# Kernel tuning notes

Hardware: AMD Instinct MI355X
Metric: run time of the kernel (lower is better)

Reference implementation:

```python
import jax, jax.numpy as jnp
import numpy as np

E, B, C, M, H = 8, 2, 1024, 2048, 7168


def setup_inputs() -> dict:
    key = jax.random.key(0)
    k1, k2, k3, k4 = jax.random.split(key, 4)
    # kaiming_uniform-ish scale for weights (bound = sqrt(6/fan_in)/sqrt(1+5) ~ 1/sqrt(fan_in))
    s_in = 1.0 / np.sqrt(M)
    s_ffn = 1.0 / np.sqrt(H)
    return {
        "dispatch_input": jax.random.normal(k1, (E, B, C, M), dtype=jnp.float32),
        "w1": jax.random.uniform(k2, (E, M, H), dtype=jnp.float32, minval=-s_in, maxval=s_in),
        "w2": jax.random.uniform(k3, (E, H, M), dtype=jnp.float32, minval=-s_ffn, maxval=s_ffn),
        "w3": jax.random.uniform(k4, (E, M, H), dtype=jnp.float32, minval=-s_in, maxval=s_in),
    }


def reference(dispatch_input, w1, w2, w3):
    # Batched per-expert SwiGLU MLP.
    # gate: [E,B,C,H], up: [E,B,C,H]
    gate = jnp.einsum("ebcm,emh->ebch", dispatch_input, w1)
    up = jnp.einsum("ebcm,emh->ebch", dispatch_input, w3)
    hidden = jax.nn.silu(gate) * up
    out = jnp.einsum("ebch,ehm->ebcm", hidden, w2)
    return out
```

## Files before the change

### kernel.cpp

```cpp
#include <hip/hip_runtime.h>

typedef __attribute__((ext_vector_type(8))) short bf16x8;
typedef __attribute__((ext_vector_type(4))) float f32x4;
typedef __attribute__((ext_vector_type(4))) unsigned int u32x4;
typedef __attribute__((ext_vector_type(4))) unsigned short u16x4;

#define NE 8
#define NT 2048
#define NM 2048
#define NH 7168

#define BAR() asm volatile("s_barrier" ::: "memory")
#define WAITV(N) asm volatile("s_waitcnt vmcnt(" #N ")" ::: "memory")

__device__ __forceinline__ unsigned short f2bf(float f) {
    unsigned int u = __float_as_uint(f);
    return (unsigned short)((u + 0x7fffu + ((u >> 16) & 1u)) >> 16);
}

__device__ __forceinline__ void gld16(const void* g, void* l) {
    __builtin_amdgcn_global_load_lds(
        (const __attribute__((address_space(1))) void*)g,
        (__attribute__((address_space(3))) void*)l, 16, 0, 0);
}


__global__ __launch_bounds__(256) void convert_x_kernel(
        const float* __restrict__ in, unsigned short* __restrict__ out) {
    const int i = blockIdx.x * 256 + threadIdx.x;
    f32x4 a = ((const f32x4*)in)[i];
    ((u16x4*)out)[i] = (u16x4){f2bf(a[0]), f2bf(a[1]), f2bf(a[2]), f2bf(a[3])};
}

__global__ __launch_bounds__(256) void convert_wT_kernel(
        const float* __restrict__ in, unsigned short* __restrict__ out,
        int R, int C) {
    const int t = threadIdx.x;
    const int e = blockIdx.y;
    const int tiles_c = C >> 6;
    const int tr = blockIdx.x / tiles_c, tc = blockIdx.x % tiles_c;

    const float* ip = in + (size_t)e * R * C + (size_t)(tr * 64) * C + tc * 64;
    unsigned short* op = out + (size_t)e * R * C + (size_t)(tc * 64) * R + tr * 64;

    __shared__ unsigned short tl[64][68];

    const int rr = t >> 4, c4 = (t & 15) * 4;
#pragma unroll
    for (int q = 0; q < 4; ++q) {
        const int r = q * 16 + rr;
        f32x4 v = *(const f32x4*)(ip + (size_t)r * C + c4);
        *(u16x4*)&tl[r][c4] = (u16x4){f2bf(v[0]), f2bf(v[1]), f2bf(v[2]), f2bf(v[3])};
    }
    __syncthreads();
#pragma unroll
    for (int q = 0; q < 4; ++q) {
        const int oc = q * 16 + rr;
        u16x4 v = (u16x4){tl[c4][oc], tl[c4 + 1][oc], tl[c4 + 2][oc], tl[c4 + 3][oc]};
        *(u16x4*)(op + (size_t)oc * R + c4) = v;
    }
}

__global__ __launch_bounds__(256) void convert_w13_kernel(
        const float* __restrict__ w1, const float* __restrict__ w3,
        unsigned short* __restrict__ wcat) {
    const int t = threadIdx.x;
    const int e = blockIdx.y;
    const int tiles_c = NH >> 6;
    const int tr = blockIdx.x / tiles_c, tc = blockIdx.x % tiles_c;

    __shared__ unsigned short tl[64][68];
    const int rr = t >> 4, c4 = (t & 15) * 4;
    unsigned short* ob = wcat + (size_t)e * (2 * NH) * NM + (size_t)(tc * 128) * NM + tr * 64;

#pragma unroll
    for (int pass = 0; pass < 2; ++pass) {
        const float* ip = (pass ? w3 : w1) + (size_t)e * NM * NH + (size_t)(tr * 64) * NH + tc * 64;
        if (pass) __syncthreads();
#pragma unroll
        for (int q = 0; q < 4; ++q) {
            const int r = q * 16 + rr;
            f32x4 v = *(const f32x4*)(ip + (size_t)r * NH + c4);
            *(u16x4*)&tl[r][c4] = (u16x4){f2bf(v[0]), f2bf(v[1]), f2bf(v[2]), f2bf(v[3])};
        }
        __syncthreads();
#pragma unroll
        for (int q = 0; q < 4; ++q) {
            const int oc = q * 16 + rr;
            const int orow = ((oc >> 4) * 32) + pass * 16 + (oc & 15);
            u16x4 v = (u16x4){tl[c4][oc], tl[c4 + 1][oc], tl[c4 + 2][oc], tl[c4 + 3][oc]};
            *(u16x4*)(ob + (size_t)orow * NM + c4) = v;
        }
    }
}

__global__ __launch_bounds__(512, 2) void gemm1p_kernel(
        const unsigned short* __restrict__ xb, const unsigned short* __restrict__ wcat,
        unsigned short* __restrict__ hid) {
    const int tid = threadIdx.x;
    const int lane = tid & 63, wv = tid >> 6;
    const int wr = wv >> 2, wc = wv & 3;
    const int e = blockIdx.y;
    const int d = blockIdx.x;
    const int l = (d & 7) * 56 + (d >> 3);
    const int ct = l >> 3, tt = l & 7;

    const unsigned short* ag = xb   + (size_t)(e * NT + tt * 256) * NM;
    const unsigned short* bg = wcat + (size_t)e * (2 * NH) * NM + (size_t)(ct * 256) * NM;
    unsigned short* hg = hid + (size_t)(e * NT + tt * 256) * NH + ct * 128;

    __shared__ __align__(16) unsigned short lds[2 * 32768];

    const int frow = lane & 15;
    const int fks  = (lane >> 4) * 8;
    const int la   = lane * 8;
    const int lr   = lane & 15, lq = lane >> 4;

    f32x4 acc[8][4];
#pragma unroll
    for (int m = 0; m < 8; ++m)
#pragma unroll
        for (int n = 0; n < 4; ++n) acc[m][n] = (f32x4){0.f, 0.f, 0.f, 0.f};

    auto stageA = [&](int t, int kh, int buf) {
        unsigned short* dst = lds + buf * 32768 + (kh * 16 + wv) * 512;
        const unsigned short* src = ag + (size_t)(wv * 16 + frow) * NM + t * 64 + kh * 32 + fks;
        gld16(src, dst);
        gld16(src + (size_t)128 * NM, dst + 8 * 512);
    };
    auto stageB = [&](int t, int kh, int buf) {
        unsigned short* dst = lds + buf * 32768 + 16384 + (kh * 16 + wv) * 512;
        const unsigned short* src = bg + (size_t)(wv * 16 + frow) * NM + t * 64 + kh * 32 + fks;
        gld16(src, dst);
        gld16(src + (size_t)128 * NM, dst + 8 * 512);
    };

    const int NKT = NM / 64;
    stageA(0, 0, 0); stageB(0, 0, 0); stageA(0, 1, 0); stageB(0, 1, 0);
    WAITV(4); BAR();

    for (int t = 0; t < NKT; ++t) {
        const int buf = t & 1, nb = buf ^ 1;
        const bool more = (t + 1 < NKT);
        const unsigned short* bA = lds + buf * 32768;
        const unsigned short* bB = bA + 16384;
        bf16x8 af[4], bfr[4];

#pragma unroll
        for (int m = 0; m < 4; ++m) af[m] = *(const bf16x8*)(bA + (wr * 8 + m) * 512 + la);
#pragma unroll
        for (int n = 0; n < 4; ++n) bfr[n] = *(const bf16x8*)(bB + (wc * 4 + n) * 512 + la);
        if (more) stageA(t + 1, 0, nb);
        BAR();
        __builtin_amdgcn_s_setprio(1);
#pragma unroll
        for (int m = 0; m < 4; ++m)
#pragma unroll
            for (int n = 0; n < 4; ++n)
                acc[m][n] = __builtin_amdgcn_mfma_f32_16x16x32_bf16(af[m], bfr[n], acc[m][n], 0, 0, 0);
        __builtin_amdgcn_s_setprio(0);
        BAR();

#pragma unroll
        for (int m = 0; m < 4; ++m) af[m] = *(const bf16x8*)(bA + (wr * 8 + 4 + m) * 512 + la);
        if (more) stageB(t + 1, 0, nb);
        BAR();
        __builtin_amdgcn_s_setprio(1);
#pragma unroll
        for (int m = 0; m < 4; ++m)
#pragma unroll
            for (int n = 0; n < 4; ++n)
                acc[4 + m][n] = __builtin_amdgcn_mfma_f32_16x16x32_bf16(af[m], bfr[n], acc[4 + m][n], 0, 0, 0);
        __builtin_amdgcn_s_setprio(0);
        if (more) { WAITV(4); } else { WAITV(0); }
        BAR();

#pragma unroll
        for (int m = 0; m < 4; ++m) af[m] = *(const bf16x8*)(bA + (16 + wr * 8 + m) * 512 + la);
#pragma unroll
        for (int n = 0; n < 4; ++n) bfr[n] = *(const bf16x8*)(bB + (16 + wc * 4 + n) * 512 + la);
        if (more) stageA(t + 1, 1, nb);
        BAR();
        __builtin_amdgcn_s_setprio(1);
#pragma unroll
        for (int m = 0; m < 4; ++m)
#pragma unroll
            for (int n = 0; n < 4; ++n)
                acc[m][n] = __builtin_amdgcn_mfma_f32_16x16x32_bf16(af[m], bfr[n], acc[m][n], 0, 0, 0);
        __builtin_amdgcn_s_setprio(0);
        BAR();

#pragma unroll
        for (int m = 0; m < 4; ++m) af[m] = *(const bf16x8*)(bA + (16 + wr * 8 + 4 + m) * 512 + la);
        if (more) stageB(t + 1, 1, nb);
        BAR();
        __builtin_amdgcn_s_setprio(1);
#pragma unroll
        for (int m = 0; m < 4; ++m)
#pragma unroll
            for (int n = 0; n < 4; ++n)
                acc[4 + m][n] = __builtin_amdgcn_mfma_f32_16x16x32_bf16(af[m], bfr[n], acc[4 + m][n], 0, 0, 0);
        __builtin_amdgcn_s_setprio(0);
        if (more) { WAITV(4); }
        BAR();
    }

#pragma unroll
    for (int mf = 0; mf < 8; ++mf)
#pragma unroll
        for (int p = 0; p < 2; ++p)
#pragma unroll
            for (int i = 0; i < 4; ++i) {
                const float g = acc[mf][2 * p][i];
                const float u = acc[mf][2 * p + 1][i];
                const float s = g / (1.f + __expf(-g));
                const int r = wr * 128 + mf * 16 + lq * 4 + i;
                const int h = wc * 32 + p * 16 + lr;
                hg[(size_t)r * NH + h] = f2bf(s * u);
            }
}

__global__ __launch_bounds__(512, 2) void gemm2p_kernel(
        const unsigned short* __restrict__ hid, const unsigned short* __restrict__ w2t,
        float* __restrict__ out) {
    const int tid = threadIdx.x;
    const int lane = tid & 63, wv = tid >> 6;
    const int wr = wv >> 2, wc = wv & 3;
    const int e = blockIdx.y;
    const int d = blockIdx.x;
    const int l = (d & 7) * 8 + (d >> 3);
    const int mt = l >> 3, tt = l & 7;

    const unsigned short* ag = hid + (size_t)(e * NT + tt * 256) * NH;
    const unsigned short* bg = w2t + (size_t)e * NM * NH + (size_t)(mt * 256) * NH;
    float* og = out + (size_t)(e * NT + tt * 256) * NM + mt * 256;

    __shared__ __align__(16) unsigned short lds[2 * 32768];

    const int frow = lane & 15;
    const int fks  = (lane >> 4) * 8;
    const int la   = lane * 8;
    const int lr   = lane & 15, lq = lane >> 4;

    f32x4 acc[8][4];
#pragma unroll
    for (int m = 0; m < 8; ++m)
#pragma unroll
        for (int n = 0; n < 4; ++n) acc[m][n] = (f32x4){0.f, 0.f, 0.f, 0.f};

    auto stageA = [&](int t, int kh, int buf) {
        unsigned short* dst = lds + buf * 32768 + (kh * 16 + wv) * 512;
        const unsigned short* src = ag + (size_t)(wv * 16 + frow) * NH + t * 64 + kh * 32 + fks;
        gld16(src, dst);
        gld16(src + (size_t)128 * NH, dst + 8 * 512);
    };
    auto stageB = [&](int t, int kh, int buf) {
        unsigned short* dst = lds + buf * 32768 + 16384 + (kh * 16 + wv) * 512;
        const unsigned short* src = bg + (size_t)(wv * 16 + frow) * NH + t * 64 + kh * 32 + fks;
        gld16(src, dst);
        gld16(src + (size_t)128 * NH, dst + 8 * 512);
    };

    const int NKT = NH / 64;
    stageA(0, 0, 0); stageB(0, 0, 0); stageA(0, 1, 0); stageB(0, 1, 0);
    WAITV(4); BAR();

    for (int t = 0; t < NKT; ++t) {
        const int buf = t & 1, nb = buf ^ 1;
        const bool more = (t + 1 < NKT);
        const unsigned short* bA = lds + buf * 32768;
        const unsigned short* bB = bA + 16384;
        bf16x8 af[4], bfr[4];

#pragma unroll
        for (int m = 0; m < 4; ++m) af[m] = *(const bf16x8*)(bA + (wr * 8 + m) * 512 + la);
#pragma unroll
        for (int n = 0; n < 4; ++n) bfr[n] = *(const bf16x8*)(bB + (wc * 4 + n) * 512 + la);
        if (more) stageA(t + 1, 0, nb);
        BAR();
        __builtin_amdgcn_s_setprio(1);
#pragma unroll
        for (int m = 0; m < 4; ++m)
#pragma unroll
            for (int n = 0; n < 4; ++n)
                acc[m][n] = __builtin_amdgcn_mfma_f32_16x16x32_bf16(af[m], bfr[n], acc[m][n], 0, 0, 0);
        __builtin_amdgcn_s_setprio(0);
        BAR();

#pragma unroll
        for (int m = 0; m < 4; ++m) af[m] = *(const bf16x8*)(bA + (wr * 8 + 4 + m) * 512 + la);
        if (more) stageB(t + 1, 0, nb);
        BAR();
        __builtin_amdgcn_s_setprio(1);
#pragma unroll
        for (int m = 0; m < 4; ++m)
#pragma unroll
            for (int n = 0; n < 4; ++n)
                acc[4 + m][n] = __builtin_amdgcn_mfma_f32_16x16x32_bf16(af[m], bfr[n], acc[4 + m][n], 0, 0, 0);
        __builtin_amdgcn_s_setprio(0);
        if (more) { WAITV(4); } else { WAITV(0); }
        BAR();

#pragma unroll
        for (int m = 0; m < 4; ++m) af[m] = *(const bf16x8*)(bA + (16 + wr * 8 + m) * 512 + la);
#pragma unroll
        for (int n = 0; n < 4; ++n) bfr[n] = *(const bf16x8*)(bB + (16 + wc * 4 + n) * 512 + la);
        if (more) stageA(t + 1, 1, nb);
        BAR();
        __builtin_amdgcn_s_setprio(1);
#pragma unroll
        for (int m = 0; m < 4; ++m)
#pragma unroll
            for (int n = 0; n < 4; ++n)
                acc[m][n] = __builtin_amdgcn_mfma_f32_16x16x32_bf16(af[m], bfr[n], acc[m][n], 0, 0, 0);
        __builtin_amdgcn_s_setprio(0);
        BAR();

#pragma unroll
        for (int m = 0; m < 4; ++m) af[m] = *(const bf16x8*)(bA + (16 + wr * 8 + 4 + m) * 512 + la);
        if (more) stageB(t + 1, 1, nb);
        BAR();
        __builtin_amdgcn_s_setprio(1);
#pragma unroll
        for (int m = 0; m < 4; ++m)
#pragma unroll
            for (int n = 0; n < 4; ++n)
                acc[4 + m][n] = __builtin_amdgcn_mfma_f32_16x16x32_bf16(af[m], bfr[n], acc[4 + m][n], 0, 0, 0);
        __builtin_amdgcn_s_setprio(0);
        if (more) { WAITV(4); }
        BAR();
    }

#pragma unroll
    for (int mf = 0; mf < 8; ++mf)
#pragma unroll
        for (int n = 0; n < 4; ++n)
#pragma unroll
            for (int i = 0; i < 4; ++i) {
                const int r = wr * 128 + mf * 16 + lq * 4 + i;
                const int c = wc * 64 + n * 16 + lr;
                og[(size_t)r * NM + c] = acc[mf][n][i];
            }
}

#define ROWB 80
#define TILEB (128 * ROWB)

__global__ __launch_bounds__(256, 2) void gemm1_fb_kernel(
        const float* __restrict__ x, const float* __restrict__ w1,
        const float* __restrict__ w3, unsigned short* __restrict__ hid) {
    const int tid = threadIdx.x;
    const int e = blockIdx.y;
    const int d = blockIdx.x;
    const int l = (d & 7) * 112 + (d >> 3);
    const int hn = l >> 4, tm = l & 15;

    const float* xg  = x  + (size_t)(e * NT + tm * 128) * NM;
    const float* w1g = w1 + (size_t)e * NM * NH + hn * 128;
    const float* w3g = w3 + (size_t)e * NM * NH + hn * 128;
    unsigned short* hg = hid + (size_t)(e * NT + tm * 128) * NH + hn * 128;

    __shared__ __align__(16) unsigned char lds[2 * 3 * TILEB];

    const int a_r = tid >> 3, a_c4 = tid & 7;
    const int w_kq = (tid >> 2) & 7;
    const int w_cg = ((tid >> 5) << 2) | (tid & 3);

    const int lane = tid & 63;
    const int wv = tid >> 6;
    const int r0w = (wv >> 1) * 64, c0w = (wv & 1) * 64;
    const int lr = lane & 15, lq = lane >> 4;

    f32x4 accg[4][4], accu[4][4];
#pragma unroll
    for (int m = 0; m < 4; ++m)
#pragma unroll
        for (int n = 0; n < 4; ++n) {
            accg[m][n] = (f32x4){0.f, 0.f, 0.f, 0.f};
            accu[m][n] = (f32x4){0.f, 0.f, 0.f, 0.f};
        }

    f32x4 la0, la1, la2, la3;
    f32x4 l10, l11, l12, l13, l30, l31, l32, l33;

    auto stage_load = [&](int ks) {
        const int k0 = ks * 32;
        const float* pa = xg + (size_t)a_r * NM + k0 + a_c4 * 4;
        la0 = *(const f32x4*)(pa);
        la1 = *(const f32x4*)(pa + 32 * NM);
        la2 = *(const f32x4*)(pa + 64 * NM);
        la3 = *(const f32x4*)(pa + 96 * NM);
        const float* p1 = w1g + (size_t)(k0 + w_kq * 4) * NH + w_cg * 4;
        l10 = *(const f32x4*)(p1);
        l11 = *(const f32x4*)(p1 + NH);
        l12 = *(const f32x4*)(p1 + 2 * NH);
        l13 = *(const f32x4*)(p1 + 3 * NH);
        const float* p3 = w3g + (size_t)(k0 + w_kq * 4) * NH + w_cg * 4;
        l30 = *(const f32x4*)(p3);
        l31 = *(const f32x4*)(p3 + NH);
        l32 = *(const f32x4*)(p3 + 2 * NH);
        l33 = *(const f32x4*)(p3 + 3 * NH);
    };

    auto stage_write = [&](int buf) {
        unsigned char* base = lds + buf * (3 * TILEB);
        unsigned char* pa = base + a_r * ROWB + a_c4 * 8;
        *(u16x4*)(pa)             = (u16x4){f2bf(la0[0]), f2bf(la0[1]), f2bf(la0[2]), f2bf(la0[3])};
        *(u16x4*)(pa + 32 * ROWB) = (u16x4){f2bf(la1[0]), f2bf(la1[1]), f2bf(la1[2]), f2bf(la1[3])};
        *(u16x4*)(pa + 64 * ROWB) = (u16x4){f2bf(la2[0]), f2bf(la2[1]), f2bf(la2[2]), f2bf(la2[3])};
        *(u16x4*)(pa + 96 * ROWB) = (u16x4){f2bf(la3[0]), f2bf(la3[1]), f2bf(la3[2]), f2bf(la3[3])};
        unsigned char* pw1 = base + TILEB + w_kq * 8;
#pragma unroll
        for (int j = 0; j < 4; ++j) {
            const int c = w_cg * 4 + j;
            *(u16x4*)(pw1 + c * ROWB) =
                (u16x4){f2bf(l10[j]), f2bf(l11[j]), f2bf(l12[j]), f2bf(l13[j])};
        }
        unsigned char* pw3 = base + 2 * TILEB + w_kq * 8;
#pragma unroll
        for (int j = 0; j < 4; ++j) {
            const int c = w_cg * 4 + j;
            *(u16x4*)(pw3 + c * ROWB) =
                (u16x4){f2bf(l30[j]), f2bf(l31[j]), f2bf(l32[j]), f2bf(l33[j])};
        }
    };

    auto compute = [&](int buf) {
        const unsigned char* base = lds + buf * (3 * TILEB);
        bf16x8 af[4], b1f[4], b3f[4];
#pragma unroll
        for (int m = 0; m < 4; ++m)
            af[m] = *(const bf16x8*)(base + (r0w + m * 16 + lr) * ROWB + lq * 16);
#pragma unroll
        for (int n = 0; n < 4; ++n) {
            b1f[n] = *(const bf16x8*)(base + TILEB + (c0w + n * 16 + lr) * ROWB + lq * 16);
            b3f[n] = *(const bf16x8*)(base + 2 * TILEB + (c0w + n * 16 + lr) * ROWB + lq * 16);
        }
#pragma unroll
        for (int m = 0; m < 4; ++m)
#pragma unroll
            for (int n = 0; n < 4; ++n) {
                accg[m][n] = __builtin_amdgcn_mfma_f32_16x16x32_bf16(af[m], b1f[n], accg[m][n], 0, 0, 0);
                accu[m][n] = __builtin_amdgcn_mfma_f32_16x16x32_bf16(af[m], b3f[n], accu[m][n], 0, 0, 0);
            }
    };

    stage_load(0);
    stage_write(0);
    __syncthreads();
    int cur = 0;
    const int NK = NM / 32;
    for (int ks = 0; ks < NK; ++ks) {
        const bool more = (ks + 1 < NK);
        if (more) stage_load(ks + 1);
        compute(cur);
        if (more) {
            stage_write(cur ^ 1);
            __syncthreads();
        }
        cur ^= 1;
    }

#pragma unroll
    for (int m = 0; m < 4; ++m)
#pragma unroll
        for (int n = 0; n < 4; ++n)
#pragma unroll
            for (int i = 0; i < 4; ++i) {
                const float g = accg[m][n][i];
                const float u = accu[m][n][i];
                const float s = g / (1.f + __expf(-g));
                const int r = r0w + m * 16 + lq * 4 + i;
                const int c = c0w + n * 16 + lr;
                hg[(size_t)r * NH + c] = f2bf(s * u);
            }
}

__global__ __launch_bounds__(256, 2) void gemm2_fb_kernel(
        const unsigned short* __restrict__ hid, const float* __restrict__ w2,
        float* __restrict__ out) {
    const int tid = threadIdx.x;
    const int e = blockIdx.y;
    const int d = blockIdx.x;
    const int l = (d & 7) * 32 + (d >> 3);
    const int mn = l >> 4, tm = l & 15;

    const unsigned short* ag = hid + (size_t)(e * NT + tm * 128) * NH;
    const float* wg = w2 + (size_t)e * NH * NM + mn * 128;
    float* og = out + (size_t)(e * NT + tm * 128) * NM + mn * 128;

    __shared__ __align__(16) unsigned char lds[2 * 2 * TILEB];

    const int a_row = tid >> 2, a_ch = tid & 3;
    const int w_kq = (tid >> 2) & 7;
    const int w_cg = ((tid >> 5) << 2) | (tid & 3);

    const int lane = tid & 63;
    const int wv = tid >> 6;
    const int r0w = (wv >> 1) * 64, c0w = (wv & 1) * 64;
    const int lr = lane & 15, lq = lane >> 4;

    f32x4 acc[4][4];
#pragma unroll
    for (int m = 0; m < 4; ++m)
#pragma unroll
        for (int n = 0; n < 4; ++n) acc[m][n] = (f32x4){0.f, 0.f, 0.f, 0.f};

    u32x4 lau0, lau1;
    f32x4 lw0, lw1, lw2, lw3;

    auto stage_load = [&](int ks) {
        const int k0 = ks * 32;
        lau0 = *(const u32x4*)(ag + (size_t)a_row * NH + k0 + a_ch * 8);
        lau1 = *(const u32x4*)(ag + (size_t)(a_row + 64) * NH + k0 + a_ch * 8);
        const float* p = wg + (size_t)(k0 + w_kq * 4) * NM + w_cg * 4;
        lw0 = *(const f32x4*)(p);
        lw1 = *(const f32x4*)(p + NM);
        lw2 = *(const f32x4*)(p + 2 * NM);
        lw3 = *(const f32x4*)(p + 3 * NM);
    };

    auto stage_write = [&](int buf) {
        unsigned char* base = lds + buf * (2 * TILEB);
        *(u32x4*)(base + a_row * ROWB + a_ch * 16) = lau0;
        *(u32x4*)(base + (a_row + 64) * ROWB + a_ch * 16) = lau1;
        unsigned char* pw = base + TILEB + w_kq * 8;
#pragma unroll
        for (int j = 0; j < 4; ++j) {
            const int c = w_cg * 4 + j;
            *(u16x4*)(pw + c * ROWB) =
                (u16x4){f2bf(lw0[j]), f2bf(lw1[j]), f2bf(lw2[j]), f2bf(lw3[j])};
        }
    };

    auto compute = [&](int buf) {
        const unsigned char* base = lds + buf * (2 * TILEB);
        bf16x8 af[4], bf[4];
#pragma unroll
        for (int m = 0; m < 4; ++m)
            af[m] = *(const bf16x8*)(base + (r0w + m * 16 + lr) * ROWB + lq * 16);
#pragma unroll
        for (int n = 0; n < 4; ++n)
            bf[n] = *(const bf16x8*)(base + TILEB + (c0w + n * 16 + lr) * ROWB + lq * 16);
#pragma unroll
        for (int m = 0; m < 4; ++m)
#pragma unroll
            for (int n = 0; n < 4; ++n)
                acc[m][n] = __builtin_amdgcn_mfma_f32_16x16x32_bf16(af[m], bf[n], acc[m][n], 0, 0, 0);
    };

    stage_load(0);
    stage_write(0);
    __syncthreads();
    int cur = 0;
    const int NK = NH / 32;
    for (int ks = 0; ks < NK; ++ks) {
        const bool more = (ks + 1 < NK);
        if (more) stage_load(ks + 1);
        compute(cur);
        if (more) {
            stage_write(cur ^ 1);
            __syncthreads();
        }
        cur ^= 1;
    }

#pragma unroll
    for (int m = 0; m < 4; ++m)
#pragma unroll
        for (int n = 0; n < 4; ++n)
#pragma unroll
            for (int i = 0; i < 4; ++i) {
                const int r = r0w + m * 16 + lq * 4 + i;
                const int c = c0w + n * 16 + lr;
                og[(size_t)r * NM + c] = acc[m][n][i];
            }
}


extern "C" void kernel_launch(void* const* d_in, const int* in_sizes, int n_in,
                              void* d_out, int out_size, void* d_ws, size_t ws_size,
                              hipStream_t stream) {
    const float* x  = (const float*)d_in[0];
    const float* w1 = (const float*)d_in[1];
    const float* w2 = (const float*)d_in[2];
    const float* w3 = (const float*)d_in[3];
    float* out = (float*)d_out;

    const size_t XB_SZ   = (size_t)NE * NT * NM * 2;
    const size_t WCAT_SZ = (size_t)NE * 2 * NH * NM * 2;
    const size_t HID_SZ  = (size_t)NE * NT * NH * 2;
    const size_t NEED = XB_SZ + WCAT_SZ + HID_SZ;

    if (ws_size >= NEED) {
        unsigned char* ws = (unsigned char*)d_ws;
        unsigned short* xbp  = (unsigned short*)(ws);
        unsigned short* wcat = (unsigned short*)(ws + XB_SZ);
        unsigned short* hidb = (unsigned short*)(ws + XB_SZ + WCAT_SZ);
        unsigned short* w2t  = (unsigned short*)(ws);

        convert_x_kernel<<<dim3((NE * NT * NM) / 1024), 256, 0, stream>>>(x, xbp);
        convert_w13_kernel<<<dim3((NM / 64) * (NH / 64), NE), 256, 0, stream>>>(w1, w3, wcat);
        gemm1p_kernel<<<dim3(448, NE), 512, 0, stream>>>(xbp, wcat, hidb);
        convert_wT_kernel<<<dim3((NH / 64) * (NM / 64), NE), 256, 0, stream>>>(w2, w2t, NH, NM);
        gemm2p_kernel<<<dim3(64, NE), 512, 0, stream>>>(hidb, w2t, out);
    } else {
        unsigned short* hid = (unsigned short*)d_ws;
        gemm1_fb_kernel<<<dim3(896, NE), 256, 0, stream>>>(x, w1, w3, hid);
        gemm2_fb_kernel<<<dim3(256, NE), 256, 0, stream>>>(hid, w2, out);
    }
}
```

Baseline: 1.952 ms.

## Pre-tile operands into MFMA fragment layout and fold w2 transpose into gemm1

Converts x, w1/w3, w2 and the hidden activations into a fragment-tiled layout so each global-to-LDS load reads contiguous 1KB chunks instead of strided rows. When the workspace is large enough, the w2 transpose/convert runs as extra blocks of the gemm1 launch, so it overlaps the first GEMM and one launch goes away. This needs extra workspace for a separate w2t buffer. The added blocks share gemm1's 512-thread launch configuration and can compete with the GEMM tiles for CU slots.

```diff
diff --git a/kernel.cpp b/kernel.cpp
--- a/kernel.cpp
+++ b/kernel.cpp
@@ -27,38 +27,20 @@
 
 __global__ __launch_bounds__(256) void convert_x_kernel(
         const float* __restrict__ in, unsigned short* __restrict__ out) {
-    const int i = blockIdx.x * 256 + threadIdx.x;
-    f32x4 a = ((const f32x4*)in)[i];
-    ((u16x4*)out)[i] = (u16x4){f2bf(a[0]), f2bf(a[1]), f2bf(a[2]), f2bf(a[3])};
-}
-
-__global__ __launch_bounds__(256) void convert_wT_kernel(
-        const float* __restrict__ in, unsigned short* __restrict__ out,
-        int R, int C) {
-    const int t = threadIdx.x;
-    const int e = blockIdx.y;
-    const int tiles_c = C >> 6;
-    const int tr = blockIdx.x / tiles_c, tc = blockIdx.x % tiles_c;
-
-    const float* ip = in + (size_t)e * R * C + (size_t)(tr * 64) * C + tc * 64;
-    unsigned short* op = out + (size_t)e * R * C + (size_t)(tc * 64) * R + tr * 64;
-
-    __shared__ unsigned short tl[64][68];
-
-    const int rr = t >> 4, c4 = (t & 15) * 4;
-#pragma unroll
-    for (int q = 0; q < 4; ++q) {
-        const int r = q * 16 + rr;
-        f32x4 v = *(const f32x4*)(ip + (size_t)r * C + c4);
-        *(u16x4*)&tl[r][c4] = (u16x4){f2bf(v[0]), f2bf(v[1]), f2bf(v[2]), f2bf(v[3])};
-    }
-    __syncthreads();
-#pragma unroll
-    for (int q = 0; q < 4; ++q) {
-        const int oc = q * 16 + rr;
-        u16x4 v = (u16x4){tl[c4][oc], tl[c4 + 1][oc], tl[c4 + 2][oc], tl[c4 + 3][oc]};
-        *(u16x4*)(op + (size_t)oc * R + c4) = v;
-    }
+    const int s = blockIdx.x * 256 + threadIdx.x;
+    const int l = s & 63;
+    const int f = (s >> 6) & 15;
+    const int t = (s >> 10) & 63;
+    const int tt = (s >> 16) & 7;
+    const int e = s >> 19;
+    const int tok = tt * 256 + f * 16 + (l & 15);
+    const int k = t * 32 + (l >> 4) * 8;
+    const float* p = in + (size_t)(e * NT + tok) * NM + k;
+    f32x4 a = *(const f32x4*)p;
+    f32x4 b = *(const f32x4*)(p + 4);
+    unsigned short* o = out + (size_t)s * 8;
+    *(u16x4*)o       = (u16x4){f2bf(a[0]), f2bf(a[1]), f2bf(a[2]), f2bf(a[3])};
+    *(u16x4*)(o + 4) = (u16x4){f2bf(b[0]), f2bf(b[1]), f2bf(b[2]), f2bf(b[3])};
 }
 
 __global__ __launch_bounds__(256) void convert_w13_kernel(
@@ -67,11 +49,11 @@
     const int t = threadIdx.x;
     const int e = blockIdx.y;
     const int tiles_c = NH >> 6;
-    const int tr = blockIdx.x / tiles_c, tc = blockIdx.x % tiles_c;
+    const int tr = blockIdx.x / tiles_c;
+    const int tc = blockIdx.x % tiles_c;
 
     __shared__ unsigned short tl[64][68];
     const int rr = t >> 4, c4 = (t & 15) * 4;
-    unsigned short* ob = wcat + (size_t)e * (2 * NH) * NM + (size_t)(tc * 128) * NM + tr * 64;
 
 #pragma unroll
     for (int pass = 0; pass < 2; ++pass) {
@@ -84,37 +66,85 @@
             *(u16x4*)&tl[r][c4] = (u16x4){f2bf(v[0]), f2bf(v[1]), f2bf(v[2]), f2bf(v[3])};
         }
         __syncthreads();
+        const int gk = tr * 64 + c4;
+        const int tk = gk >> 5, krun = (gk >> 3) & 3, j = gk & 7;
 #pragma unroll
         for (int q = 0; q < 4; ++q) {
             const int oc = q * 16 + rr;
-            const int orow = ((oc >> 4) * 32) + pass * 16 + (oc & 15);
+            const int gh = tc * 64 + oc;
+            const int ct = gh >> 7;
+            const int fh = (((gh >> 4) & 7) << 1) + pass;
+            const int lp = gh & 15;
             u16x4 v = (u16x4){tl[c4][oc], tl[c4 + 1][oc], tl[c4 + 2][oc], tl[c4 + 3][oc]};
-            *(u16x4*)(ob + (size_t)orow * NM + c4) = v;
-        }
-    }
+            unsigned short* dst = wcat + ((((size_t)(e * 56 + ct) * 64 + tk) * 16 + fh) << 9)
+                                  + (lp + (krun << 4)) * 8 + j;
+            *(u16x4*)dst = v;
+        }
+    }
+}
+
+__device__ __forceinline__ void w2_transpose_tile(
+        const float* __restrict__ w2, unsigned short* __restrict__ w2t,
+        int e, int tile, int t, unsigned short (*tl)[68]) {
+    const int tr = tile >> 5;
+    const int tc = tile & 31;
+    const float* ip = w2 + (size_t)e * NH * NM + (size_t)(tr * 64) * NM + tc * 64;
+    const int rr = t >> 4, c4 = (t & 15) * 4;
+#pragma unroll
+    for (int q = 0; q < 4; ++q) {
+        const int r = q * 16 + rr;
+        f32x4 v = *(const f32x4*)(ip + (size_t)r * NM + c4);
+        *(u16x4*)&tl[r][c4] = (u16x4){f2bf(v[0]), f2bf(v[1]), f2bf(v[2]), f2bf(v[3])};
+    }
+    __syncthreads();
+    const int gh = tr * 64 + c4;
+    const int tk = gh >> 5, krun = (gh >> 3) & 3, j = gh & 7;
+#pragma unroll
+    for (int q = 0; q < 4; ++q) {
+        const int oc = q * 16 + rr;
+        const int gm = tc * 64 + oc;
+        const int mt = gm >> 8, fm = (gm >> 4) & 15, lp = gm & 15;
+        u16x4 v = (u16x4){tl[c4][oc], tl[c4 + 1][oc], tl[c4 + 2][oc], tl[c4 + 3][oc]};
+        unsigned short* dst = w2t + ((((size_t)(e * 8 + mt) * 224 + tk) * 16 + fm) << 9)
+                              + (lp + (krun << 4)) * 8 + j;
+        *(u16x4*)dst = v;
+    }
+}
+
+__global__ __launch_bounds__(256) void convert_w2t_kernel(
+        const float* __restrict__ w2, unsigned short* __restrict__ w2t) {
+    __shared__ unsigned short tl[64][68];
+    w2_transpose_tile(w2, w2t, blockIdx.y, blockIdx.x, threadIdx.x, tl);
 }
 
 __global__ __launch_bounds__(512, 2) void gemm1p_kernel(
         const unsigned short* __restrict__ xb, const unsigned short* __restrict__ wcat,
-        unsigned short* __restrict__ hid) {
+        unsigned short* __restrict__ hid,
+        const float* __restrict__ w2, unsigned short* __restrict__ w2t) {
     const int tid = threadIdx.x;
+    const int e = blockIdx.y;
+    const int d = blockIdx.x;
+
+    __shared__ __align__(16) unsigned short lds[2 * 32768];
+
+    if (d >= 448) {
+        const int tile = (d - 448) * 2 + (tid >> 8);
+        unsigned short (*tl)[68] = (unsigned short (*)[68])(lds + (tid >> 8) * 4352);
+        w2_transpose_tile(w2, w2t, e, tile, tid & 255, tl);
+        return;
+    }
+
     const int lane = tid & 63, wv = tid >> 6;
     const int wr = wv >> 2, wc = wv & 3;
-    const int e = blockIdx.y;
-    const int d = blockIdx.x;
     const int l = (d & 7) * 56 + (d >> 3);
     const int ct = l >> 3, tt = l & 7;
 
-    const unsigned short* ag = xb   + (size_t)(e * NT + tt * 256) * NM;
-    const unsigned short* bg = wcat + (size_t)e * (2 * NH) * NM + (size_t)(ct * 256) * NM;
-    unsigned short* hg = hid + (size_t)(e * NT + tt * 256) * NH + ct * 128;
-
-    __shared__ __align__(16) unsigned short lds[2 * 32768];
-
-    const int frow = lane & 15;
-    const int fks  = (lane >> 4) * 8;
-    const int la   = lane * 8;
-    const int lr   = lane & 15, lq = lane >> 4;
+    const unsigned short* ag = xb   + (size_t)(e * 8 + tt) * 64 * 8192;
+    const unsigned short* bg = wcat + (size_t)(e * 56 + ct) * 64 * 8192;
+    unsigned short* hb = hid + (size_t)(e * 8 + tt) * 224 * 8192;
+
+    const int la = lane * 8;
+    const int lr = lane & 15, lq = lane >> 4;
 
     f32x4 acc[8][4];
 #pragma unroll
@@ -124,15 +154,15 @@
 
     auto stageA = [&](int t, int kh, int buf) {
         unsigned short* dst = lds + buf * 32768 + (kh * 16 + wv) * 512;
-        const unsigned short* src = ag + (size_t)(wv * 16 + frow) * NM + t * 64 + kh * 32 + fks;
+        const unsigned short* src = ag + (((size_t)(2 * t + kh) * 16 + wv) << 9) + la;
         gld16(src, dst);
-        gld16(src + (size_t)128 * NM, dst + 8 * 512);
+        gld16(src + 8 * 512, dst + 8 * 512);
     };
     auto stageB = [&](int t, int kh, int buf) {
         unsigned short* dst = lds + buf * 32768 + 16384 + (kh * 16 + wv) * 512;
-        const unsigned short* src = bg + (size_t)(wv * 16 + frow) * NM + t * 64 + kh * 32 + fks;
+        const unsigned short* src = bg + (((size_t)(2 * t + kh) * 16 + wv) << 9) + la;
         gld16(src, dst);
-        gld16(src + (size_t)128 * NM, dst + 8 * 512);
+        gld16(src + 8 * 512, dst + 8 * 512);
     };
 
     const int NKT = NM / 64;
@@ -205,19 +235,23 @@
         BAR();
     }
 
-#pragma unroll
-    for (int mf = 0; mf < 8; ++mf)
-#pragma unroll
-        for (int p = 0; p < 2; ++p)
-#pragma unroll
-            for (int i = 0; i < 4; ++i) {
-                const float g = acc[mf][2 * p][i];
-                const float u = acc[mf][2 * p + 1][i];
-                const float s = g / (1.f + __expf(-g));
-                const int r = wr * 128 + mf * 16 + lq * 4 + i;
-                const int h = wc * 32 + p * 16 + lr;
-                hg[(size_t)r * NH + h] = f2bf(s * u);
-            }
+    {
+        unsigned short* hb2 = hb + (((size_t)(ct * 4 + wc) * 16) << 9);
+        const int jj = lr & 7;
+#pragma unroll
+        for (int mf = 0; mf < 8; ++mf)
+#pragma unroll
+            for (int p = 0; p < 2; ++p)
+#pragma unroll
+                for (int i = 0; i < 4; ++i) {
+                    const float g = acc[mf][2 * p][i];
+                    const float u = acc[mf][2 * p + 1][i];
+                    const float s = g / (1.f + __expf(-g));
+                    const int fidx = wr * 8 + mf;
+                    const int lidx = (lq * 4 + i) + ((p * 2 + (lr >> 3)) << 4);
+                    hb2[((size_t)fidx << 9) + lidx * 8 + jj] = f2bf(s * u);
+                }
+    }
 }
 
 __global__ __launch_bounds__(512, 2) void gemm2p_kernel(
@@ -231,16 +265,14 @@
     const int l = (d & 7) * 8 + (d >> 3);
     const int mt = l >> 3, tt = l & 7;
 
-    const unsigned short* ag = hid + (size_t)(e * NT + tt * 256) * NH;
-    const unsigned short* bg = w2t + (size_t)e * NM * NH + (size_t)(mt * 256) * NH;
+    const unsigned short* ag = hid + (size_t)(e * 8 + tt) * 224 * 8192;
+    const unsigned short* bg = w2t + (size_t)(e * 8 + mt) * 224 * 8192;
     float* og = out + (size_t)(e * NT + tt * 256) * NM + mt * 256;
 
     __shared__ __align__(16) unsigned short lds[2 * 32768];
 
-    const int frow = lane & 15;
-    const int fks  = (lane >> 4) * 8;
-    const int la   = lane * 8;
-    const int lr   = lane & 15, lq = lane >> 4;
+    const int la = lane * 8;
+    const int lr = lane & 15, lq = lane >> 4;
 
     f32x4 acc[8][4];
 #pragma unroll
@@ -250,15 +282,15 @@
 
     auto stageA = [&](int t, int kh, int buf) {
         unsigned short* dst = lds + buf * 32768 + (kh * 16 + wv) * 512;
-        const unsigned short* src = ag + (size_t)(wv * 16 + frow) * NH + t * 64 + kh * 32 + fks;
+        const unsigned short* src = ag + (((size_t)(2 * t + kh) * 16 + wv) << 9) + la;
         gld16(src, dst);
-        gld16(src + (size_t)128 * NH, dst + 8 * 512);
+        gld16(src + 8 * 512, dst + 8 * 512);
     };
     auto stageB = [&](int t, int kh, int buf) {
         unsigned short* dst = lds + buf * 32768 + 16384 + (kh * 16 + wv) * 512;
-        const unsigned short* src = bg + (size_t)(wv * 16 + frow) * NH + t * 64 + kh * 32 + fks;
+        const unsigned short* src = bg + (((size_t)(2 * t + kh) * 16 + wv) << 9) + la;
         gld16(src, dst);
-        gld16(src + (size_t)128 * NH, dst + 8 * 512);
+        gld16(src + 8 * 512, dst + 8 * 512);
     };
 
     const int NKT = NH / 64;
@@ -590,19 +622,32 @@
     const size_t XB_SZ   = (size_t)NE * NT * NM * 2;
     const size_t WCAT_SZ = (size_t)NE * 2 * NH * NM * 2;
     const size_t HID_SZ  = (size_t)NE * NT * NH * 2;
-    const size_t NEED = XB_SZ + WCAT_SZ + HID_SZ;
-
-    if (ws_size >= NEED) {
-        unsigned char* ws = (unsigned char*)d_ws;
+    const size_t W2T_SZ  = (size_t)NE * NM * NH * 2;
+    const size_t NEED_FULL = XB_SZ + WCAT_SZ + HID_SZ + W2T_SZ;
+    const size_t NEED_STD  = XB_SZ + WCAT_SZ + HID_SZ;
+
+    unsigned char* ws = (unsigned char*)d_ws;
+
+    if (ws_size >= NEED_FULL) {
+        unsigned short* xbp  = (unsigned short*)(ws);
+        unsigned short* wcat = (unsigned short*)(ws + XB_SZ);
+        unsigned short* hidb = (unsigned short*)(ws + XB_SZ + WCAT_SZ);
+        unsigned short* w2t  = (unsigned short*)(ws + XB_SZ + WCAT_SZ + HID_SZ);
+
+        convert_x_kernel<<<dim3((NE * NT * NM / 8) / 256), 256, 0, stream>>>(x, xbp);
+        convert_w13_kernel<<<dim3((NM / 64) * (NH / 64), NE), 256, 0, stream>>>(w1, w3, wcat);
+        gemm1p_kernel<<<dim3(448 + 1792, NE), 512, 0, stream>>>(xbp, wcat, hidb, w2, w2t);
+        gemm2p_kernel<<<dim3(64, NE), 512, 0, stream>>>(hidb, w2t, out);
+    } else if (ws_size >= NEED_STD) {
         unsigned short* xbp  = (unsigned short*)(ws);
         unsigned short* wcat = (unsigned short*)(ws + XB_SZ);
         unsigned short* hidb = (unsigned short*)(ws + XB_SZ + WCAT_SZ);
         unsigned short* w2t  = (unsigned short*)(ws);
 
-        convert_x_kernel<<<dim3((NE * NT * NM) / 1024), 256, 0, stream>>>(x, xbp);
+        convert_x_kernel<<<dim3((NE * NT * NM / 8) / 256), 256, 0, stream>>>(x, xbp);
         convert_w13_kernel<<<dim3((NM / 64) * (NH / 64), NE), 256, 0, stream>>>(w1, w3, wcat);
-        gemm1p_kernel<<<dim3(448, NE), 512, 0, stream>>>(xbp, wcat, hidb);
-        convert_wT_kernel<<<dim3((NH / 64) * (NM / 64), NE), 256, 0, stream>>>(w2, w2t, NH, NM);
+        gemm1p_kernel<<<dim3(448, NE), 512, 0, stream>>>(xbp, wcat, hidb, w2, w2t);
+        convert_w2t_kernel<<<dim3((NH / 64) * (NM / 64), NE), 256, 0, stream>>>(w2, w2t);
         gemm2p_kernel<<<dim3(64, NE), 512, 0, stream>>>(hidb, w2t, out);
     } else {
         unsigned short* hid = (unsigned short*)d_ws;
```

After: 1.664 ms. 1.17x faster.
